# Optimization experiments

Hardware: AMD Instinct MI355X
Metric: run time of the kernel (lower is better)

Reference implementation:

```python
import jax, jax.numpy as jnp
import numpy as np

# ---- module hyperparameters (from init_kwargs) ----
K_CURV = 1.0      # Lorentz curvature k
MAX_NORM = 1000.0 # rescale_to_max cap on space-norm (assumed)
KSIZE = 5
STRIDE = 2
PAD = 2
IN_CH = 257       # includes time dim -> 256 space channels
OUT_CH = 257
LIN_FEATS = (IN_CH - 1) * KSIZE + 1  # 1281
EPS = 1e-8


def _add_time(space):
    # time = sqrt(k + ||space||^2), concat on last axis
    time = jnp.sqrt(K_CURV + jnp.sum(space * space, axis=-1, keepdims=True))
    return jnp.concatenate([time, space], axis=-1)


def _rescale_to_max(x):
    # clamp space-norm to MAX_NORM, then recompute valid time component
    space = x[..., 1:]
    norm = jnp.sqrt(jnp.sum(space * space, axis=-1, keepdims=True))
    scale = jnp.minimum(1.0, MAX_NORM / jnp.maximum(norm, EPS))
    return _add_time(space * scale)


def setup_inputs() -> dict:
    key = jax.random.key(0)
    kx, kw, kb = jax.random.split(key, 3)
    x = jax.random.normal(kx, (16, 8192, IN_CH), dtype=jnp.float32)
    W = jax.random.normal(kw, (OUT_CH, LIN_FEATS), dtype=jnp.float32) * 0.02
    b = jax.random.normal(kb, (OUT_CH,), dtype=jnp.float32) * 0.01
    return {"x": x, "W": W, "b": b}


def reference(x, W, b):
    B, L, C = x.shape
    # pad length dim with zeros (time channel of padded frames is clamped in
    # torch, but the time channel is discarded before add_time, so only the
    # space channels matter)
    xp = jnp.pad(x, ((0, 0), (PAD, PAD), (0, 0)))
    space = xp[..., 1:]                                  # (B, Lp, C-1)
    Lp = L + 2 * PAD
    n_frames = (Lp - KSIZE) // STRIDE + 1
    # im2col gather: (n_frames, K) window indices
    idx = jnp.arange(n_frames)[:, None] * STRIDE + jnp.arange(KSIZE)[None, :]
    patches = space[:, idx, :]                           # (B, n, K, C-1)
    # torch reorders to kernel-major (k, c) layout before add_time
    ps = patches.reshape(B, n_frames, KSIZE * (C - 1))   # (B, n, K*(C-1))
    pk = _add_time(ps)                                   # (B, n, lin_feats)
    out = jnp.einsum('bnf,of->bno', pk, W) + b           # LorentzProjection
    out = _add_time(out[..., 1:])                        # manifold.projx
    out = _rescale_to_max(out)                           # rescale_after=True
    return out
```

## Files before the change

kernel.cpp:

```cpp
#include <hip/hip_runtime.h>
#include <hip/hip_bf16.h>
#include <cstdint>
#include <cstddef>

namespace {

constexpr int BATCH = 16;
constexpr int LEN   = 8192;
constexpr int CIN   = 257;
constexpr int CS    = 256;
constexpr int NF    = 4096;
constexpr int LPAD  = LEN + 4;
constexpr int KG    = 1280;
constexpr int MT    = 128;

constexpr size_t XS_ELEMS  = (size_t)BATCH * LPAD * CS;
constexpr size_t XS_BYTES  = XS_ELEMS * 2;
constexpr size_t RSQ_OFF   = XS_BYTES;
constexpr size_t RSQ_BYTES = (size_t)BATCH * LPAD * 4;
constexpr size_t WT_OFF    = RSQ_OFF + RSQ_BYTES;
constexpr size_t WT_BYTES  = (size_t)CS * KG * 2;
constexpr size_t W0_OFF    = WT_OFF + WT_BYTES;
constexpr size_t WS_NEED   = W0_OFF + (size_t)CS * 4;

typedef __attribute__((ext_vector_type(8))) short short8;
typedef __attribute__((ext_vector_type(8))) unsigned short ushort8v;
typedef __attribute__((ext_vector_type(4))) float f32x4;

__device__ __forceinline__ unsigned short f2bf_bits(float f) {
  union { __hip_bfloat16 h; unsigned short u; } cv;
  cv.h = __float2bfloat16(f);
  return cv.u;
}

__device__ __forceinline__ void async_cp16(const void* g, void* l) {
  __builtin_amdgcn_global_load_lds(
      (const __attribute__((address_space(1))) void*)g,
      (__attribute__((address_space(3))) void*)l,
      16, 0, 0);
}

}

__global__ void prep_w_kernel(const float* __restrict__ W,
                              __hip_bfloat16* __restrict__ wt,
                              float* __restrict__ w0) {
  int n = blockIdx.x;
  const float* wrow = W + (size_t)(n + 1) * 1281;
  for (int k = threadIdx.x; k < KG; k += blockDim.x)
    wt[(size_t)n * KG + k] = __float2bfloat16(wrow[1 + k]);
  if (threadIdx.x == 0) w0[n] = wrow[0];
}

__global__ void prep_x_kernel(const float* __restrict__ x,
                              __hip_bfloat16* __restrict__ xs,
                              float* __restrict__ rowsq) {
  const int tid = threadIdx.x;
  const int bx  = blockIdx.x;
  if (bx < 8192) {
    __shared__ float4 xf4[1028];
    const float4* src = (const float4*)(x + (size_t)bx * 4112);
#pragma unroll
    for (int i = 0; i < 4; ++i) {
      int idx = i * 256 + tid;
      xf4[idx] = src[idx];
    }
    if (tid < 4) xf4[1024 + tid] = src[1024 + tid];
    __syncthreads();
    const float* xf = (const float*)xf4;
    const int row = tid >> 4, seg = tid & 15;
    const float* v = xf + row * 257 + 1 + seg * 16;
    float ss = 0.f;
    unsigned short u[16];
#pragma unroll
    for (int i = 0; i < 16; ++i) {
      float f = v[i];
      ss += f * f;
      u[i] = f2bf_bits(f);
    }
    const int b = bx >> 9;
    const int t = (bx & 511) * 16 + row;
    const size_t tpg = (size_t)b * LPAD + 2 + t;
    ushort8v* dst = (ushort8v*)((unsigned short*)xs + tpg * CS + seg * 16);
    ushort8v p0, p1;
#pragma unroll
    for (int i = 0; i < 8; ++i) { p0[i] = u[i]; p1[i] = u[8 + i]; }
    dst[0] = p0;
    dst[1] = p1;
    ss += __shfl_xor(ss, 1);
    ss += __shfl_xor(ss, 2);
    ss += __shfl_xor(ss, 4);
    ss += __shfl_xor(ss, 8);
    if (seg == 0) rowsq[tpg] = ss;
  } else {
    for (int i = tid; i < 64 * 128; i += 256) {
      int row = i >> 7, uo = i & 127;
      int b = row >> 2, j = row & 3;
      size_t tpg = (size_t)b * LPAD + (j < 2 ? j : 8192 + j);
      ((uint32_t*)xs)[tpg * 128 + uo] = 0;
      if (uo == 0) rowsq[tpg] = 0.0f;
    }
  }
}

__global__ __launch_bounds__(512, 4) void lorentz_gemm_kernel(
    const __hip_bfloat16* __restrict__ xs,
    const __hip_bfloat16* __restrict__ wt,
    const float* __restrict__ rowsq,
    const float* __restrict__ w0,
    const float* __restrict__ bvec,
    float* __restrict__ out) {
  __shared__ alignas(16) char lds[16384 + 32768];
  __shared__ alignas(16) float time0_s[128];
  __shared__ alignas(16) float normsq_s[128];
  char* A_lds = lds;
  char* B_lds = lds + 16384;

  const int tid   = threadIdx.x;
  const int w     = tid >> 6;
  const int lane  = tid & 63;
  const int row16 = lane & 15;
  const int q     = lane >> 4;
  const int mh    = w >> 2;
  const int nq    = w & 3;

  const int bx    = blockIdx.x;
  const int b     = bx >> 5;
  const int Mblk  = (bx & 31) * MT;

  const __hip_bfloat16* xsb = xs + ((size_t)b * LPAD + 2 * Mblk) * CS;

  f32x4 acc[4][4];
#pragma unroll
  for (int i = 0; i < 4; ++i)
#pragma unroll
    for (int j = 0; j < 4; ++j) acc[i][j] = (f32x4){0.f, 0.f, 0.f, 0.f};

  const int csw = (lane & 7) ^ (lane >> 3);

  for (int it = 0; it < 20; ++it) {
    const int kk = it >> 2;
    const int c0 = (it & 3) << 6;
    const int k0 = it << 6;
    __syncthreads();
#pragma unroll
    for (int j = 0; j < 2; ++j) {
      int m = w * 16 + j * 8 + (lane >> 3);
      const void* g = xsb + (size_t)(2 * m + kk) * CS + c0 + csw * 8;
      async_cp16(g, A_lds + (w * 2 + j) * 1024);
    }
#pragma unroll
    for (int j = 0; j < 4; ++j) {
      int n = w * 32 + j * 8 + (lane >> 3);
      const void* g = wt + (size_t)n * KG + k0 + csw * 8;
      async_cp16(g, B_lds + (w * 4 + j) * 1024);
    }
    __syncthreads();
#pragma unroll
    for (int s = 0; s < 2; ++s) {
      const int p = (s * 4 + q) ^ (lane & 7);
      short8 bfr[4];
#pragma unroll
      for (int nt = 0; nt < 4; ++nt)
        bfr[nt] = *(const short8*)(B_lds + ((nq * 64 + nt * 16 + row16) * 8 + p) * 16);
#pragma unroll
      for (int mt = 0; mt < 4; ++mt) {
        short8 af = *(const short8*)(A_lds + ((mh * 64 + mt * 16 + row16) * 8 + p) * 16);
#pragma unroll
        for (int nt = 0; nt < 4; ++nt)
          acc[mt][nt] = __builtin_amdgcn_mfma_f32_16x16x32_bf16(
              af, bfr[nt], acc[mt][nt], 0, 0, 0);
      }
    }
  }

  __syncthreads();
  if (tid < 128) {
    const float* rs = rowsq + (size_t)b * LPAD + 2 * (Mblk + tid);
    float s5 = rs[0] + rs[1] + rs[2] + rs[3] + rs[4];
    time0_s[tid] = sqrtf(1.0f + s5);
    normsq_s[tid] = 0.0f;
  }
  __syncthreads();

  float w0v[4], bv[4];
#pragma unroll
  for (int nt = 0; nt < 4; ++nt) {
    int n = nq * 64 + nt * 16 + row16;
    w0v[nt] = w0[n];
    bv[nt]  = bvec[1 + n];
  }

#pragma unroll
  for (int mt = 0; mt < 4; ++mt) {
    f32x4 t4 = *(const f32x4*)&time0_s[mh * 64 + mt * 16 + q * 4];
#pragma unroll
    for (int nt = 0; nt < 4; ++nt)
#pragma unroll
      for (int r = 0; r < 4; ++r)
        acc[mt][nt][r] = acc[mt][nt][r] + t4[r] * w0v[nt] + bv[nt];
#pragma unroll
    for (int r = 0; r < 4; ++r) {
      float ps = 0.f;
#pragma unroll
      for (int nt = 0; nt < 4; ++nt) ps += acc[mt][nt][r] * acc[mt][nt][r];
      ps += __shfl_xor(ps, 1);
      ps += __shfl_xor(ps, 2);
      ps += __shfl_xor(ps, 4);
      ps += __shfl_xor(ps, 8);
      if (row16 == 0) atomicAdd(&normsq_s[mh * 64 + mt * 16 + q * 4 + r], ps);
    }
  }
  __syncthreads();

#pragma unroll
  for (int mt = 0; mt < 4; ++mt) {
#pragma unroll
    for (int r = 0; r < 4; ++r) {
      int m = mh * 64 + mt * 16 + q * 4 + r;
      float nsq  = normsq_s[m];
      float norm = sqrtf(nsq);
      float scale = fminf(1.0f, 1000.0f / fmaxf(norm, 1e-8f));
      size_t ob = ((size_t)b * NF + Mblk + m) * 257;
#pragma unroll
      for (int nt = 0; nt < 4; ++nt) {
        int n = nq * 64 + nt * 16 + row16;
        out[ob + 1 + n] = acc[mt][nt][r] * scale;
      }
    }
  }
  if (tid < 128) {
    float nsq  = normsq_s[tid];
    float norm = sqrtf(nsq);
    float scale = fminf(1.0f, 1000.0f / fmaxf(norm, 1e-8f));
    size_t ob = ((size_t)b * NF + Mblk + tid) * 257;
    out[ob] = sqrtf(1.0f + scale * scale * nsq);
  }
}

__global__ void fallback_kernel(const float* __restrict__ x,
                                const float* __restrict__ W,
                                const float* __restrict__ bvec,
                                float* __restrict__ out) {
  int fid = blockIdx.x;
  int b = fid >> 12;
  int g = fid & (NF - 1);
  __shared__ float patch[1280];
  __shared__ float red[256];
  int tid = threadIdx.x;
  float ss = 0.f;
  for (int k = tid; k < 1280; k += 256) {
    int kk = k >> 8, c = k & 255;
    int t = 2 * g + kk - 2;
    float v = (t >= 0 && t < LEN) ? x[((size_t)b * LEN + t) * CIN + 1 + c] : 0.f;
    patch[k] = v;
    ss += v * v;
  }
  red[tid] = ss;
  __syncthreads();
  for (int off = 128; off > 0; off >>= 1) {
    if (tid < off) red[tid] += red[tid + off];
    __syncthreads();
  }
  float time0 = sqrtf(1.f + red[0]);
  __syncthreads();
  const float* wrow = W + (size_t)(tid + 1) * 1281;
  float acc = time0 * wrow[0] + bvec[tid + 1];
  for (int k = 0; k < 1280; ++k) acc += wrow[1 + k] * patch[k];
  red[tid] = acc * acc;
  __syncthreads();
  for (int off = 128; off > 0; off >>= 1) {
    if (tid < off) red[tid] += red[tid + off];
    __syncthreads();
  }
  float nsq = red[0];
  float norm = sqrtf(nsq);
  float scale = fminf(1.f, 1000.f / fmaxf(norm, 1e-8f));
  size_t ob = ((size_t)b * NF + g) * 257;
  out[ob + 1 + tid] = acc * scale;
  if (tid == 0) out[ob] = sqrtf(1.f + scale * scale * nsq);
}

extern "C" void kernel_launch(void* const* d_in, const int* in_sizes, int n_in,
                              void* d_out, int out_size, void* d_ws, size_t ws_size,
                              hipStream_t stream) {
  const float* x  = (const float*)d_in[0];
  const float* W  = (const float*)d_in[1];
  const float* bv = (const float*)d_in[2];
  float* out = (float*)d_out;

  if (ws_size >= WS_NEED) {
    char* ws = (char*)d_ws;
    __hip_bfloat16* xs = (__hip_bfloat16*)ws;
    float* rowsq       = (float*)(ws + RSQ_OFF);
    __hip_bfloat16* wt = (__hip_bfloat16*)(ws + WT_OFF);
    float* w0          = (float*)(ws + W0_OFF);
    prep_w_kernel<<<256, 256, 0, stream>>>(W, wt, w0);
    prep_x_kernel<<<8193, 256, 0, stream>>>(x, xs, rowsq);
    lorentz_gemm_kernel<<<BATCH * (NF / MT), 512, 0, stream>>>(xs, wt, rowsq, w0, bv, out);
  } else {
    fallback_kernel<<<BATCH * NF, 256, 0, stream>>>(x, W, bv, out);
  }
}
```

Baseline: 272.3 us.

## Stage whole A window in LDS once, stream pre-packed W fragments from global

The GEMM kernel now loads the block's entire 136-row input strip into swizzled LDS with a single async copy up front, which removes the per-iteration double syncthreads. W is pre-packed by the prep kernel into MFMA fragment order, so each wave reads its B operands straight from global/L2 into registers. A three-deep register pipeline prefetches A and B two k-steps ahead. The block shrinks to 64 rows and 4 waves, with each wave covering 64 output columns. The trade-offs are more W traffic from L2 per block and higher register pressure.

```diff
diff --git a/kernel.cpp b/kernel.cpp
--- a/kernel.cpp
+++ b/kernel.cpp
@@ -11,17 +11,17 @@
 constexpr int CS    = 256;
 constexpr int NF    = 4096;
 constexpr int LPAD  = LEN + 4;
-constexpr int KG    = 1280;
-constexpr int MT    = 128;
-
-constexpr size_t XS_ELEMS  = (size_t)BATCH * LPAD * CS;
-constexpr size_t XS_BYTES  = XS_ELEMS * 2;
+constexpr int NKS   = 40;
+constexpr int MT    = 64;
+
+constexpr int    XS_ROWS   = BATCH * LPAD;
+constexpr size_t XS_BYTES  = (size_t)(XS_ROWS + 16) * 512;
 constexpr size_t RSQ_OFF   = XS_BYTES;
-constexpr size_t RSQ_BYTES = (size_t)BATCH * LPAD * 4;
-constexpr size_t WT_OFF    = RSQ_OFF + RSQ_BYTES;
-constexpr size_t WT_BYTES  = (size_t)CS * KG * 2;
-constexpr size_t W0_OFF    = WT_OFF + WT_BYTES;
-constexpr size_t WS_NEED   = W0_OFF + (size_t)CS * 4;
+constexpr size_t RSQ_BYTES = (size_t)XS_ROWS * 4;
+constexpr size_t WPK_OFF   = RSQ_OFF + RSQ_BYTES;
+constexpr size_t WPK_BYTES = (size_t)16 * NKS * 64 * 8 * 2;
+constexpr size_t W0_OFF    = WPK_OFF + WPK_BYTES + 4096;
+constexpr size_t WS_NEED   = W0_OFF + 1024;
 
 typedef __attribute__((ext_vector_type(8))) short short8;
 typedef __attribute__((ext_vector_type(8))) unsigned short ushort8v;
@@ -43,13 +43,20 @@
 }
 
 __global__ void prep_w_kernel(const float* __restrict__ W,
-                              __hip_bfloat16* __restrict__ wt,
+                              __hip_bfloat16* __restrict__ wpk,
                               float* __restrict__ w0) {
-  int n = blockIdx.x;
-  const float* wrow = W + (size_t)(n + 1) * 1281;
-  for (int k = threadIdx.x; k < KG; k += blockDim.x)
-    wt[(size_t)n * KG + k] = __float2bfloat16(wrow[1 + k]);
-  if (threadIdx.x == 0) w0[n] = wrow[0];
+  int t = blockIdx.x * 256 + threadIdx.x;
+  int lane = t & 63;
+  int ks   = (t >> 6) % NKS;
+  int nf   = t / (NKS * 64);
+  int n    = nf * 16 + (lane & 15);
+  int kh   = lane >> 4;
+  const float* src = W + (size_t)(n + 1) * 1281 + 1 + ks * 32 + kh * 8;
+  ushort8v pk;
+#pragma unroll
+  for (int j = 0; j < 8; ++j) pk[j] = f2bf_bits(src[j]);
+  *(ushort8v*)(wpk + (size_t)t * 8) = pk;
+  if (t < 256) w0[t] = W[(size_t)(t + 1) * 1281];
 }
 
 __global__ void prep_x_kernel(const float* __restrict__ x,
@@ -103,32 +110,36 @@
   }
 }
 
-__global__ __launch_bounds__(512, 4) void lorentz_gemm_kernel(
+__global__ __launch_bounds__(256, 2) void lorentz_gemm_kernel(
     const __hip_bfloat16* __restrict__ xs,
-    const __hip_bfloat16* __restrict__ wt,
+    const __hip_bfloat16* __restrict__ wpk,
     const float* __restrict__ rowsq,
     const float* __restrict__ w0,
     const float* __restrict__ bvec,
     float* __restrict__ out) {
-  __shared__ alignas(16) char lds[16384 + 32768];
-  __shared__ alignas(16) float time0_s[128];
-  __shared__ alignas(16) float normsq_s[128];
-  char* A_lds = lds;
-  char* B_lds = lds + 16384;
+  __shared__ alignas(16) char A_lds[136 * 512];
+  __shared__ alignas(16) float time0_s[64];
+  __shared__ alignas(16) float normsq_s[64];
 
   const int tid   = threadIdx.x;
   const int w     = tid >> 6;
   const int lane  = tid & 63;
   const int row16 = lane & 15;
   const int q     = lane >> 4;
-  const int mh    = w >> 2;
-  const int nq    = w & 3;
 
   const int bx    = blockIdx.x;
-  const int b     = bx >> 5;
-  const int Mblk  = (bx & 31) * MT;
-
-  const __hip_bfloat16* xsb = xs + ((size_t)b * LPAD + 2 * Mblk) * CS;
+  const int b     = bx >> 6;
+  const int Mblk  = (bx & 63) * MT;
+
+  const char* xsb = (const char*)(xs + ((size_t)b * LPAD + 2 * Mblk) * CS);
+
+#pragma unroll
+  for (int j = 0; j < 17; ++j) {
+    int cid = (j * 4 + w) * 64 + lane;
+    int r = cid >> 5, c = cid & 31;
+    int sw = (r >> 1) & 15;
+    async_cp16(xsb + r * 512 + ((c ^ sw) << 4), (char*)A_lds + cid * 16);
+  }
 
   f32x4 acc[4][4];
 #pragma unroll
@@ -136,46 +147,49 @@
 #pragma unroll
     for (int j = 0; j < 4; ++j) acc[i][j] = (f32x4){0.f, 0.f, 0.f, 0.f};
 
-  const int csw = (lane & 7) ^ (lane >> 3);
-
-  for (int it = 0; it < 20; ++it) {
-    const int kk = it >> 2;
-    const int c0 = (it & 3) << 6;
-    const int k0 = it << 6;
-    __syncthreads();
-#pragma unroll
-    for (int j = 0; j < 2; ++j) {
-      int m = w * 16 + j * 8 + (lane >> 3);
-      const void* g = xsb + (size_t)(2 * m + kk) * CS + c0 + csw * 8;
-      async_cp16(g, A_lds + (w * 2 + j) * 1024);
-    }
-#pragma unroll
-    for (int j = 0; j < 4; ++j) {
-      int n = w * 32 + j * 8 + (lane >> 3);
-      const void* g = wt + (size_t)n * KG + k0 + csw * 8;
-      async_cp16(g, B_lds + (w * 4 + j) * 1024);
-    }
-    __syncthreads();
-#pragma unroll
-    for (int s = 0; s < 2; ++s) {
-      const int p = (s * 4 + q) ^ (lane & 7);
-      short8 bfr[4];
+  const __hip_bfloat16* bb[4];
+#pragma unroll
+  for (int nt = 0; nt < 4; ++nt)
+    bb[nt] = wpk + ((size_t)(w * 4 + nt) * NKS * 64 + lane) * 8;
+
+  auto loadA = [&](short8* a, int ks) {
+    int k  = ks * 32 + q * 8;
+    int kk = k >> 8;
+    int lc = (k & 255) >> 3;
+#pragma unroll
+    for (int mt = 0; mt < 4; ++mt) {
+      int rl = mt * 32 + row16 * 2 + kk;
+      int pc = lc ^ ((rl >> 1) & 15);
+      a[mt] = *(const short8*)(A_lds + rl * 512 + pc * 16);
+    }
+  };
+  auto loadB = [&](short8* bf, int ks) {
+#pragma unroll
+    for (int nt = 0; nt < 4; ++nt)
+      bf[nt] = *(const short8*)(bb[nt] + (size_t)ks * 512);
+  };
+
+  __syncthreads();
+
+  short8 Af[3][4], Bf[3][4];
+  loadA(Af[0], 0); loadB(Bf[0], 0);
+  loadA(Af[1], 1); loadB(Bf[1], 1);
+
+#pragma unroll
+  for (int ks = 0; ks < NKS; ++ks) {
+    const int cur = ks % 3;
+    const int nxt = (ks + 2) % 3;
+    if (ks < NKS - 2) { loadB(Bf[nxt], ks + 2); loadA(Af[nxt], ks + 2); }
+#pragma unroll
+    for (int mt = 0; mt < 4; ++mt)
 #pragma unroll
       for (int nt = 0; nt < 4; ++nt)
-        bfr[nt] = *(const short8*)(B_lds + ((nq * 64 + nt * 16 + row16) * 8 + p) * 16);
-#pragma unroll
-      for (int mt = 0; mt < 4; ++mt) {
-        short8 af = *(const short8*)(A_lds + ((mh * 64 + mt * 16 + row16) * 8 + p) * 16);
-#pragma unroll
-        for (int nt = 0; nt < 4; ++nt)
-          acc[mt][nt] = __builtin_amdgcn_mfma_f32_16x16x32_bf16(
-              af, bfr[nt], acc[mt][nt], 0, 0, 0);
-      }
-    }
-  }
-
-  __syncthreads();
-  if (tid < 128) {
+        acc[mt][nt] = __builtin_amdgcn_mfma_f32_16x16x32_bf16(
+            Af[cur][mt], Bf[cur][nt], acc[mt][nt], 0, 0, 0);
+  }
+
+  __syncthreads();
+  if (tid < 64) {
     const float* rs = rowsq + (size_t)b * LPAD + 2 * (Mblk + tid);
     float s5 = rs[0] + rs[1] + rs[2] + rs[3] + rs[4];
     time0_s[tid] = sqrtf(1.0f + s5);
@@ -186,14 +200,14 @@
   float w0v[4], bv[4];
 #pragma unroll
   for (int nt = 0; nt < 4; ++nt) {
-    int n = nq * 64 + nt * 16 + row16;
+    int n = w * 64 + nt * 16 + row16;
     w0v[nt] = w0[n];
     bv[nt]  = bvec[1 + n];
   }
 
 #pragma unroll
   for (int mt = 0; mt < 4; ++mt) {
-    f32x4 t4 = *(const f32x4*)&time0_s[mh * 64 + mt * 16 + q * 4];
+    f32x4 t4 = *(const f32x4*)&time0_s[mt * 16 + q * 4];
 #pragma unroll
     for (int nt = 0; nt < 4; ++nt)
 #pragma unroll
@@ -208,7 +222,7 @@
       ps += __shfl_xor(ps, 2);
       ps += __shfl_xor(ps, 4);
       ps += __shfl_xor(ps, 8);
-      if (row16 == 0) atomicAdd(&normsq_s[mh * 64 + mt * 16 + q * 4 + r], ps);
+      if (row16 == 0) atomicAdd(&normsq_s[mt * 16 + q * 4 + r], ps);
     }
   }
   __syncthreads();
@@ -217,19 +231,19 @@
   for (int mt = 0; mt < 4; ++mt) {
 #pragma unroll
     for (int r = 0; r < 4; ++r) {
-      int m = mh * 64 + mt * 16 + q * 4 + r;
+      int m = mt * 16 + q * 4 + r;
       float nsq  = normsq_s[m];
       float norm = sqrtf(nsq);
       float scale = fminf(1.0f, 1000.0f / fmaxf(norm, 1e-8f));
       size_t ob = ((size_t)b * NF + Mblk + m) * 257;
 #pragma unroll
       for (int nt = 0; nt < 4; ++nt) {
-        int n = nq * 64 + nt * 16 + row16;
+        int n = w * 64 + nt * 16 + row16;
         out[ob + 1 + n] = acc[mt][nt][r] * scale;
       }
     }
   }
-  if (tid < 128) {
+  if (tid < 64) {
     float nsq  = normsq_s[tid];
     float norm = sqrtf(nsq);
     float scale = fminf(1.0f, 1000.0f / fmaxf(norm, 1e-8f));
@@ -291,13 +305,13 @@
 
   if (ws_size >= WS_NEED) {
     char* ws = (char*)d_ws;
-    __hip_bfloat16* xs = (__hip_bfloat16*)ws;
-    float* rowsq       = (float*)(ws + RSQ_OFF);
-    __hip_bfloat16* wt = (__hip_bfloat16*)(ws + WT_OFF);
-    float* w0          = (float*)(ws + W0_OFF);
-    prep_w_kernel<<<256, 256, 0, stream>>>(W, wt, w0);
+    __hip_bfloat16* xs  = (__hip_bfloat16*)ws;
+    float* rowsq        = (float*)(ws + RSQ_OFF);
+    __hip_bfloat16* wpk = (__hip_bfloat16*)(ws + WPK_OFF);
+    float* w0           = (float*)(ws + W0_OFF);
+    prep_w_kernel<<<160, 256, 0, stream>>>(W, wpk, w0);
     prep_x_kernel<<<8193, 256, 0, stream>>>(x, xs, rowsq);
-    lorentz_gemm_kernel<<<BATCH * (NF / MT), 512, 0, stream>>>(xs, wt, rowsq, w0, bv, out);
+    lorentz_gemm_kernel<<<BATCH * (NF / MT), 256, 0, stream>>>(xs, wpk, rowsq, w0, bv, out);
   } else {
     fallback_kernel<<<BATCH * NF, 256, 0, stream>>>(x, W, bv, out);
   }
```

After: 292.2 us. +7.3%, slower.
